# Performance work log

Measured on AMD Instinct MI355X. Metric: run time of the kernel, lower is better.

The kernel has to match this reference:

```python
import jax, jax.numpy as jnp
import numpy as np

D_MODEL = 1024
NUM_HEAD = 16


def setup_inputs() -> dict:
    key = jax.random.key(0)
    ks = jax.random.split(key, 11)
    B, S, D = 2, 2048, D_MODEL
    scale = 1.0 / np.sqrt(D)
    inp = {
        "Q": jax.random.normal(ks[0], (B, S, D), jnp.float32),
        "K": jax.random.normal(ks[1], (B, S, D), jnp.float32),
        "V": jax.random.normal(ks[2], (B, S, D), jnp.float32),
        "Wq": jax.random.normal(ks[3], (D, D), jnp.float32) * scale,
        "bq": jax.random.normal(ks[4], (D,), jnp.float32) * 0.01,
        "Wk": jax.random.normal(ks[5], (D, D), jnp.float32) * scale,
        "bk": jax.random.normal(ks[6], (D,), jnp.float32) * 0.01,
        "Wv": jax.random.normal(ks[7], (D, D), jnp.float32) * scale,
        "bv": jax.random.normal(ks[8], (D,), jnp.float32) * 0.01,
        "Wo": jax.random.normal(ks[9], (D, D), jnp.float32) * scale,
        "bo": jax.random.normal(ks[10], (D,), jnp.float32) * 0.01,
    }
    return inp


def reference(Q, K, V, Wq, bq, Wk, bk, Wv, bv, Wo, bo):
    b, vc, d_model = Q.shape
    h = NUM_HEAD
    hd = d_model // h
    # projections (torch Linear: x @ W.T + b)
    q = (Q @ Wq.T + bq).reshape(b, vc, h, hd)
    k = (K @ Wk.T + bk).reshape(b, vc, h, hd)
    v = (V @ Wv.T + bv).reshape(b, vc, h, hd)
    # scores [b,h,q,k]
    atten = jnp.einsum('bqhd,bkhd->bhqk', q, k) / np.sqrt(hd).astype(jnp.float32)
    atten = jax.nn.softmax(atten, axis=3)
    # weighted values -> [b,q,h,hd]
    out = jnp.einsum('bhqd,bdhv->bqhv', atten, v).reshape(b, vc, d_model)
    return out @ Wo.T + bo
```

## Files before the change

### kernel.cpp

```cpp
#include <hip/hip_runtime.h>

#define S_LEN 2048
#define DM 1024
#define NH 16
#define HD 64
#define NB 2

typedef unsigned short u16;
typedef __attribute__((ext_vector_type(8))) short s16x8;
typedef __attribute__((ext_vector_type(8))) unsigned short u16x8;
typedef __attribute__((ext_vector_type(4))) float fx4;
typedef __attribute__((ext_vector_type(2))) unsigned u32x2;
typedef __attribute__((ext_vector_type(4))) unsigned u32x4;

__device__ __forceinline__ u16 f2bf(float f) {
  unsigned u = __builtin_bit_cast(unsigned, f);
  return (u16)((u + 0x7FFFu + ((u >> 16) & 1u)) >> 16);
}

__device__ __forceinline__ unsigned cvt_pk_bf16(float a, float b) {
  unsigned r;
  asm("v_cvt_pk_bf16_f32 %0, %1, %2" : "=v"(r) : "v"(a), "v"(b));
  return r;
}

__device__ __forceinline__ void gload16(const void* g, void* l) {
  __builtin_amdgcn_global_load_lds(
      (const __attribute__((address_space(1))) unsigned*)g,
      (__attribute__((address_space(3))) unsigned*)l, 16, 0, 0);
}

__device__ __forceinline__ fx4 mfma16(s16x8 a, s16x8 b, fx4 c) {
  return __builtin_amdgcn_mfma_f32_16x16x32_bf16(a, b, c, 0, 0, 0);
}

__global__ __launch_bounds__(256) void cvt_w_kernel(
    const float* __restrict__ Wq, const float* __restrict__ Wk,
    const float* __restrict__ Wv, const float* __restrict__ Wo,
    u16* __restrict__ Wqb, u16* __restrict__ Wkb, u16* __restrict__ Wvb,
    u16* __restrict__ Wob) {
  const int blk = blockIdx.x;
  const float* src;
  u16* dst;
  float scale = 1.0f;
  int off;
  if (blk < 512)       { src = Wq; dst = Wqb; off = blk;        scale = 0.18033688f; }
  else if (blk < 1024) { src = Wk; dst = Wkb; off = blk - 512;  }
  else if (blk < 1536) { src = Wv; dst = Wvb; off = blk - 1024; }
  else                 { src = Wo; dst = Wob; off = blk - 1536; }
  const int i = (off * 256 + (int)threadIdx.x) * 8;
  fx4 a = *(const fx4*)(src + i);
  fx4 b = *(const fx4*)(src + i + 4);
  u16x8 o;
  o[0] = f2bf(a[0] * scale); o[1] = f2bf(a[1] * scale);
  o[2] = f2bf(a[2] * scale); o[3] = f2bf(a[3] * scale);
  o[4] = f2bf(b[0] * scale); o[5] = f2bf(b[1] * scale);
  o[6] = f2bf(b[2] * scale); o[7] = f2bf(b[3] * scale);
  *(u16x8*)(dst + i) = o;
}

__device__ __forceinline__ void store_out(u16* C, size_t idx, float v) { C[idx] = f2bf(v); }
__device__ __forceinline__ void store_out(float* C, size_t idx, float v) { C[idx] = v; }

template <typename OUT, bool AF32>
__device__ __forceinline__ void gemm_db_body(const u16* __restrict__ Abf,
                                             const float* __restrict__ Afp,
                                             const u16* __restrict__ Bt,
                                             const float* __restrict__ bias,
                                             float bscale, OUT* __restrict__ C,
                                             int m0, int n0) {
  __shared__ u16 Al[2][128 * 32];
  __shared__ u16 Bl[2][128 * 32];
  const int tid = threadIdx.x;
  const int wid = tid >> 6, lane = tid & 63;
  const int g = lane >> 4, lr = lane & 15;
  const int wr = wid >> 1, wc = wid & 1;
  const int row0 = tid >> 2, ch = tid & 3;
  const int chx = ch ^ ((row0 >> 1) & 3);
  const int wch = chx;

  fx4 acc[4][4] = {};
  fx4 pf[4];

  auto issueA = [&](int k0) {
#pragma unroll
    for (int hh = 0; hh < 2; ++hh) {
      const float* ap = Afp + (size_t)(m0 + hh * 64 + row0) * 1024 + k0 + ch * 8;
      pf[2 * hh] = *(const fx4*)ap;
      pf[2 * hh + 1] = *(const fx4*)(ap + 4);
    }
  };
  auto writeA = [&](int buf) {
#pragma unroll
    for (int hh = 0; hh < 2; ++hh) {
      u32x4 w;
      w[0] = cvt_pk_bf16(pf[2 * hh][0], pf[2 * hh][1]);
      w[1] = cvt_pk_bf16(pf[2 * hh][2], pf[2 * hh][3]);
      w[2] = cvt_pk_bf16(pf[2 * hh + 1][0], pf[2 * hh + 1][1]);
      w[3] = cvt_pk_bf16(pf[2 * hh + 1][2], pf[2 * hh + 1][3]);
      *(u32x4*)((char*)Al[buf] + hh * 4096 + row0 * 64 + wch * 16) = w;
    }
  };
  auto stage = [&](int buf, int k0) {
    if constexpr (!AF32) {
      gload16(Abf + (size_t)(m0 + row0) * 1024 + k0 + chx * 8,
              (char*)Al[buf] + wid * 1024);
      gload16(Abf + (size_t)(m0 + 64 + row0) * 1024 + k0 + chx * 8,
              (char*)Al[buf] + 4096 + wid * 1024);
    }
    gload16(Bt + (size_t)(n0 + row0) * 1024 + k0 + chx * 8,
            (char*)Bl[buf] + wid * 1024);
    gload16(Bt + (size_t)(n0 + 64 + row0) * 1024 + k0 + chx * 8,
            (char*)Bl[buf] + 4096 + wid * 1024);
  };
  auto compute = [&](int cur) {
    s16x8 a[4], b[4];
#pragma unroll
    for (int m = 0; m < 4; ++m) {
      const int row = wr * 64 + m * 16 + lr;
      a[m] = *(const s16x8*)((char*)Al[cur] + row * 64 + (g ^ ((row >> 1) & 3)) * 16);
    }
#pragma unroll
    for (int n = 0; n < 4; ++n) {
      const int row = wc * 64 + n * 16 + lr;
      b[n] = *(const s16x8*)((char*)Bl[cur] + row * 64 + (g ^ ((row >> 1) & 3)) * 16);
    }
    __builtin_amdgcn_s_setprio(1);
#pragma unroll
    for (int m = 0; m < 4; ++m)
#pragma unroll
      for (int n = 0; n < 4; ++n) acc[m][n] = mfma16(a[m], b[n], acc[m][n]);
    __builtin_amdgcn_s_setprio(0);
  };

  if constexpr (AF32) issueA(0);
  stage(0, 0);
  if constexpr (AF32) writeA(0);
  __syncthreads();

#pragma unroll 1
  for (int t = 0; t < 32; t += 2) {
    if constexpr (AF32) issueA((t + 1) * 32);
    stage(1, (t + 1) * 32);
    compute(0);
    if constexpr (AF32) writeA(1);
    __syncthreads();
    if (t + 2 < 32) {
      if constexpr (AF32) issueA((t + 2) * 32);
      stage(0, (t + 2) * 32);
    }
    compute(1);
    if (t + 2 < 32 && AF32) writeA(0);
    __syncthreads();
  }

#pragma unroll
  for (int n = 0; n < 4; ++n) {
    const int col = n0 + wc * 64 + n * 16 + lr;
    const float bv = bias[col] * bscale;
#pragma unroll
    for (int m = 0; m < 4; ++m) {
      const int row = m0 + wr * 64 + m * 16 + g * 4;
#pragma unroll
      for (int j = 0; j < 4; ++j)
        store_out(C, (size_t)(row + j) * 1024 + col, acc[m][n][j] + bv);
    }
  }
}

__global__ __launch_bounds__(256, 3) void gemm_qkv_kernel(
    const float* Q, const float* K, const float* V, const u16* Wq, const u16* Wk,
    const u16* Wv, const float* bq, const float* bk, const float* bv, u16* q,
    u16* k, u16* v) {
  const int hw = blockIdx.x + (blockIdx.y << 3) + (blockIdx.z << 8);
  const int xcd = hw & 7, j = hw >> 3;
  const int x = j & 7;
  const int p = xcd + ((j >> 3) << 3);
  const int y = p & 31, z = p >> 5;

  const float* A;
  const u16* B;
  const float* bias;
  u16* C;
  float bs;
  if (z == 0)      { A = Q; B = Wq; bias = bq; C = q; bs = 0.18033688f; }
  else if (z == 1) { A = K; B = Wk; bias = bk; C = k; bs = 1.0f; }
  else             { A = V; B = Wv; bias = bv; C = v; bs = 1.0f; }
  gemm_db_body<u16, true>(nullptr, A, B, bias, bs, C, y * 128, x * 128);
}

__global__ __launch_bounds__(256, 3) void gemm_out_kernel(const u16* ctx,
                                                          const u16* Wo,
                                                          const float* bo,
                                                          float* out) {
  const int hw = blockIdx.x + (blockIdx.y << 3);
  const int xcd = hw & 7, j = hw >> 3;
  const int x = j & 7;
  const int y = xcd + ((j >> 3) << 3);
  gemm_db_body<float, false>(ctx, nullptr, Wo, bo, 1.0f, out, y * 128, x * 128);
}

__global__ __launch_bounds__(256) void transpose_v_kernel(const u16* __restrict__ v,
                                                          u16* __restrict__ vt) {
  const int bh = blockIdx.y;
  const int b = bh >> 4, h = bh & 15;
  const int s0 = blockIdx.x * 32;
  const int d = threadIdx.x & 63;
  const int c = threadIdx.x >> 6;
  const int s = s0 + c * 8;
  const u16* src = v + ((size_t)(b * S_LEN + s)) * DM + h * HD + d;
  u16x8 o;
#pragma unroll
  for (int e = 0; e < 8; ++e) o[e] = src[(size_t)e * DM];
  *(u16x8*)(vt + ((size_t)(bh * 64 + d)) * S_LEN + s) = o;
}

__global__ __launch_bounds__(256, 4) void attn_kernel(const u16* __restrict__ qb,
                                                      const u16* __restrict__ kb,
                                                      const u16* __restrict__ vt,
                                                      u16* __restrict__ ctx) {
  __shared__ u16 Kl[2][64 * 64];
  __shared__ u16 Vl[2][64 * 64];
  __shared__ u16 Pl[4][16 * 64];

  const int tid = threadIdx.x, wid = tid >> 6, lane = tid & 63;
  const int g = lane >> 4, lr = lane & 15;
  const int rswz = (lr & 7) * 8;
  const int pswz = (lr & 7) * 16;
  char* Pb = (char*)&Pl[wid][0];
  const int bh = blockIdx.y, b = bh >> 4, h = bh & 15;
  const int q0 = blockIdx.x * 64;

  const u16* qp = qb + ((size_t)(b * S_LEN + q0 + wid * 16 + lr)) * DM + h * HD;
  s16x8 aq[2];
  aq[0] = *(const s16x8*)(qp + g * 8);
  aq[1] = *(const s16x8*)(qp + 32 + g * 8);

  fx4 accO[4] = {};
  float lrun = 0.f;

  const int srow = tid >> 3, sch = tid & 7;
  const int schx = sch ^ (srow & 7);
  const u16* kbase = kb + ((size_t)b * S_LEN) * DM + h * HD;
  const u16* vtbase = vt + ((size_t)bh * 64) * S_LEN;

#define STAGE(buf, kv)                                                             \
  do {                                                                             \
    gload16(kbase + (size_t)((kv) + srow) * DM + schx * 8,                         \
            (char*)Kl[buf] + wid * 1024);                                          \
    gload16(kbase + (size_t)((kv) + 32 + srow) * DM + schx * 8,                    \
            (char*)Kl[buf] + 4096 + wid * 1024);                                   \
    gload16(vtbase + (size_t)srow * S_LEN + (kv) + schx * 8,                       \
            (char*)Vl[buf] + wid * 1024);                                          \
    gload16(vtbase + (size_t)(32 + srow) * S_LEN + (kv) + schx * 8,                \
            (char*)Vl[buf] + 4096 + wid * 1024);                                   \
  } while (0)

  auto compute_tile = [&](const u16* Kc0, const u16* Vc0) {
    fx4 s[4] = {};
    __builtin_amdgcn_s_setprio(1);
#pragma unroll
    for (int ks = 0; ks < 2; ++ks) {
#pragma unroll
      for (int c = 0; c < 4; ++c) {
        s16x8 kf =
            *(const s16x8*)(Kc0 + (c * 16 + lr) * 64 + ((ks * 32 + g * 8) ^ rswz));
        s[c] = mfma16(kf, aq[ks], s[c]);
      }
    }
    __builtin_amdgcn_s_setprio(0);

#pragma unroll
    for (int c = 0; c < 4; ++c)
#pragma unroll
      for (int j = 0; j < 4; ++j) s[c][j] = __builtin_amdgcn_exp2f(s[c][j]);
    {
      const float r0 = (s[0][0] + s[0][1]) + (s[0][2] + s[0][3]);
      const float r1 = (s[1][0] + s[1][1]) + (s[1][2] + s[1][3]);
      const float r2 = (s[2][0] + s[2][1]) + (s[2][2] + s[2][3]);
      const float r3 = (s[3][0] + s[3][1]) + (s[3][2] + s[3][3]);
      lrun += (r0 + r1) + (r2 + r3);
    }

#pragma unroll
    for (int c = 0; c < 4; ++c) {
      u32x2 w;
      w[0] = cvt_pk_bf16(s[c][0], s[c][1]);
      w[1] = cvt_pk_bf16(s[c][2], s[c][3]);
      *(u32x2*)(Pb + lr * 128 + ((c * 32 + g * 8) ^ pswz)) = w;
    }
    asm volatile("s_waitcnt lgkmcnt(0)" ::: "memory");
    __builtin_amdgcn_sched_barrier(0);

    __builtin_amdgcn_s_setprio(1);
#pragma unroll
    for (int ks = 0; ks < 2; ++ks) {
      s16x8 pb = *(const s16x8*)(Pb + lr * 128 + ((ks * 64 + g * 16) ^ pswz));
#pragma unroll
      for (int c = 0; c < 4; ++c) {
        s16x8 vf =
            *(const s16x8*)(Vc0 + (c * 16 + lr) * 64 + ((ks * 32 + g * 8) ^ rswz));
        accO[c] = mfma16(vf, pb, accO[c]);
      }
    }
    __builtin_amdgcn_s_setprio(0);
  };

  STAGE(0, 0);
  __syncthreads();

  for (int t = 0; t < 32; t += 2) {
    if (t + 1 < 32) STAGE(1, (t + 1) * 64);
    compute_tile(Kl[0], Vl[0]);
    __syncthreads();
    if (t + 2 < 32) STAGE(0, (t + 2) * 64);
    compute_tile(Kl[1], Vl[1]);
    __syncthreads();
  }
#undef STAGE

  lrun += __shfl_xor(lrun, 16);
  lrun += __shfl_xor(lrun, 32);
  const float inv = 1.0f / lrun;
  u16* op = ctx + ((size_t)(b * S_LEN + q0 + wid * 16 + lr)) * DM + h * HD;
#pragma unroll
  for (int c = 0; c < 4; ++c) {
    u32x2 w;
    w[0] = cvt_pk_bf16(accO[c][0] * inv, accO[c][1] * inv);
    w[1] = cvt_pk_bf16(accO[c][2] * inv, accO[c][3] * inv);
    *(u32x2*)(op + c * 16 + g * 4) = w;
  }
}

extern "C" void kernel_launch(void* const* d_in, const int* in_sizes, int n_in,
                              void* d_out, int out_size, void* d_ws, size_t ws_size,
                              hipStream_t stream) {
  const float* Q = (const float*)d_in[0];
  const float* K = (const float*)d_in[1];
  const float* V = (const float*)d_in[2];
  const float* Wq = (const float*)d_in[3];
  const float* bq = (const float*)d_in[4];
  const float* Wk = (const float*)d_in[5];
  const float* bk = (const float*)d_in[6];
  const float* Wv = (const float*)d_in[7];
  const float* bv = (const float*)d_in[8];
  const float* Wo = (const float*)d_in[9];
  const float* bo = (const float*)d_in[10];
  float* out = (float*)d_out;

  char* ws = (char*)d_ws;
  const size_t SZ_T = (size_t)NB * S_LEN * DM * 2;
  const size_t SZ_W = (size_t)DM * DM * 2;

  u16* Wqb = (u16*)(ws);
  u16* Wkb = (u16*)(ws + SZ_W);
  u16* Wvb = (u16*)(ws + 2 * SZ_W);
  u16* Wob = (u16*)(ws + 3 * SZ_W);
  u16* qb  = (u16*)(ws + 4 * SZ_W);
  u16* kb  = (u16*)(ws + 4 * SZ_W + SZ_T);
  u16* vb  = (u16*)(ws + 4 * SZ_W + 2 * SZ_T);
  u16* vtb = (u16*)(ws + 4 * SZ_W + 3 * SZ_T);
  u16* ctx = (u16*)(ws + 4 * SZ_W + 4 * SZ_T);

  cvt_w_kernel<<<2048, 256, 0, stream>>>(Wq, Wk, Wv, Wo, Wqb, Wkb, Wvb, Wob);

  gemm_qkv_kernel<<<dim3(8, 32, 3), 256, 0, stream>>>(Q, K, V, Wqb, Wkb, Wvb,
                                                      bq, bk, bv, qb, kb, vb);

  transpose_v_kernel<<<dim3(64, 32), 256, 0, stream>>>(vb, vtb);

  attn_kernel<<<dim3(32, 32), 256, 0, stream>>>(qb, kb, vtb, ctx);

  gemm_out_kernel<<<dim3(8, 32), 256, 0, stream>>>(ctx, Wob, bo, out);
}
```

Baseline: 123.8 us.

## Pre-convert Q/K/V activations to bf16 in a separate pass before QKV GEMM

The QKV GEMM used to load fp32 activations through registers, convert them to bf16 and write them to LDS on every k-step. Q, K and V are now converted once in an expanded conversion kernel, so the GEMM can use direct global-to-LDS loads for both operands, as the output GEMM already does. Workspace buffers are reused for the V transpose and the context. This adds a full extra read and write pass over the activations. Separately, an explicit LDS wait and scheduling barrier in the attention kernel are removed, which may affect ordering between the P stores and the loads that follow.

```diff
diff --git a/kernel.cpp b/kernel.cpp
--- a/kernel.cpp
+++ b/kernel.cpp
@@ -11,7 +11,6 @@
 typedef __attribute__((ext_vector_type(8))) unsigned short u16x8;
 typedef __attribute__((ext_vector_type(4))) float fx4;
 typedef __attribute__((ext_vector_type(2))) unsigned u32x2;
-typedef __attribute__((ext_vector_type(4))) unsigned u32x4;
 
 __device__ __forceinline__ u16 f2bf(float f) {
   unsigned u = __builtin_bit_cast(unsigned, f);
@@ -34,20 +33,25 @@
   return __builtin_amdgcn_mfma_f32_16x16x32_bf16(a, b, c, 0, 0, 0);
 }
 
-__global__ __launch_bounds__(256) void cvt_w_kernel(
-    const float* __restrict__ Wq, const float* __restrict__ Wk,
-    const float* __restrict__ Wv, const float* __restrict__ Wo,
-    u16* __restrict__ Wqb, u16* __restrict__ Wkb, u16* __restrict__ Wvb,
-    u16* __restrict__ Wob) {
+__global__ __launch_bounds__(256) void cvt_all_kernel(
+    const float* __restrict__ Q, const float* __restrict__ K,
+    const float* __restrict__ V, const float* __restrict__ Wq,
+    const float* __restrict__ Wk, const float* __restrict__ Wv,
+    const float* __restrict__ Wo, u16* __restrict__ Qc, u16* __restrict__ Kc,
+    u16* __restrict__ Vc, u16* __restrict__ Wqb, u16* __restrict__ Wkb,
+    u16* __restrict__ Wvb, u16* __restrict__ Wob) {
   const int blk = blockIdx.x;
   const float* src;
   u16* dst;
   float scale = 1.0f;
   int off;
-  if (blk < 512)       { src = Wq; dst = Wqb; off = blk;        scale = 0.18033688f; }
-  else if (blk < 1024) { src = Wk; dst = Wkb; off = blk - 512;  }
-  else if (blk < 1536) { src = Wv; dst = Wvb; off = blk - 1024; }
-  else                 { src = Wo; dst = Wob; off = blk - 1536; }
+  if (blk < 2048)      { src = Q;  dst = Qc;  off = blk; }
+  else if (blk < 4096) { src = K;  dst = Kc;  off = blk - 2048; }
+  else if (blk < 6144) { src = V;  dst = Vc;  off = blk - 4096; }
+  else if (blk < 6656) { src = Wq; dst = Wqb; off = blk - 6144; scale = 0.18033688f; }
+  else if (blk < 7168) { src = Wk; dst = Wkb; off = blk - 6656; }
+  else if (blk < 7680) { src = Wv; dst = Wvb; off = blk - 7168; }
+  else                 { src = Wo; dst = Wob; off = blk - 7680; }
   const int i = (off * 256 + (int)threadIdx.x) * 8;
   fx4 a = *(const fx4*)(src + i);
   fx4 b = *(const fx4*)(src + i + 4);
@@ -62,9 +66,8 @@
 __device__ __forceinline__ void store_out(u16* C, size_t idx, float v) { C[idx] = f2bf(v); }
 __device__ __forceinline__ void store_out(float* C, size_t idx, float v) { C[idx] = v; }
 
-template <typename OUT, bool AF32>
-__device__ __forceinline__ void gemm_db_body(const u16* __restrict__ Abf,
-                                             const float* __restrict__ Afp,
+template <typename OUT>
+__device__ __forceinline__ void gemm_db_body(const u16* __restrict__ A,
                                              const u16* __restrict__ Bt,
                                              const float* __restrict__ bias,
                                              float bscale, OUT* __restrict__ C,
@@ -77,37 +80,14 @@
   const int wr = wid >> 1, wc = wid & 1;
   const int row0 = tid >> 2, ch = tid & 3;
   const int chx = ch ^ ((row0 >> 1) & 3);
-  const int wch = chx;
 
   fx4 acc[4][4] = {};
-  fx4 pf[4];
-
-  auto issueA = [&](int k0) {
-#pragma unroll
-    for (int hh = 0; hh < 2; ++hh) {
-      const float* ap = Afp + (size_t)(m0 + hh * 64 + row0) * 1024 + k0 + ch * 8;
-      pf[2 * hh] = *(const fx4*)ap;
-      pf[2 * hh + 1] = *(const fx4*)(ap + 4);
-    }
-  };
-  auto writeA = [&](int buf) {
-#pragma unroll
-    for (int hh = 0; hh < 2; ++hh) {
-      u32x4 w;
-      w[0] = cvt_pk_bf16(pf[2 * hh][0], pf[2 * hh][1]);
-      w[1] = cvt_pk_bf16(pf[2 * hh][2], pf[2 * hh][3]);
-      w[2] = cvt_pk_bf16(pf[2 * hh + 1][0], pf[2 * hh + 1][1]);
-      w[3] = cvt_pk_bf16(pf[2 * hh + 1][2], pf[2 * hh + 1][3]);
-      *(u32x4*)((char*)Al[buf] + hh * 4096 + row0 * 64 + wch * 16) = w;
-    }
-  };
+
   auto stage = [&](int buf, int k0) {
-    if constexpr (!AF32) {
-      gload16(Abf + (size_t)(m0 + row0) * 1024 + k0 + chx * 8,
-              (char*)Al[buf] + wid * 1024);
-      gload16(Abf + (size_t)(m0 + 64 + row0) * 1024 + k0 + chx * 8,
-              (char*)Al[buf] + 4096 + wid * 1024);
-    }
+    gload16(A + (size_t)(m0 + row0) * 1024 + k0 + chx * 8,
+            (char*)Al[buf] + wid * 1024);
+    gload16(A + (size_t)(m0 + 64 + row0) * 1024 + k0 + chx * 8,
+            (char*)Al[buf] + 4096 + wid * 1024);
     gload16(Bt + (size_t)(n0 + row0) * 1024 + k0 + chx * 8,
             (char*)Bl[buf] + wid * 1024);
     gload16(Bt + (size_t)(n0 + 64 + row0) * 1024 + k0 + chx * 8,
@@ -133,24 +113,16 @@
     __builtin_amdgcn_s_setprio(0);
   };
 
-  if constexpr (AF32) issueA(0);
   stage(0, 0);
-  if constexpr (AF32) writeA(0);
   __syncthreads();
 
 #pragma unroll 1
   for (int t = 0; t < 32; t += 2) {
-    if constexpr (AF32) issueA((t + 1) * 32);
     stage(1, (t + 1) * 32);
     compute(0);
-    if constexpr (AF32) writeA(1);
     __syncthreads();
-    if (t + 2 < 32) {
-      if constexpr (AF32) issueA((t + 2) * 32);
-      stage(0, (t + 2) * 32);
-    }
+    if (t + 2 < 32) stage(0, (t + 2) * 32);
     compute(1);
-    if (t + 2 < 32 && AF32) writeA(0);
     __syncthreads();
   }
 
@@ -169,7 +141,7 @@
 }
 
 __global__ __launch_bounds__(256, 3) void gemm_qkv_kernel(
-    const float* Q, const float* K, const float* V, const u16* Wq, const u16* Wk,
+    const u16* Qc, const u16* Kc, const u16* Vc, const u16* Wq, const u16* Wk,
     const u16* Wv, const float* bq, const float* bk, const float* bv, u16* q,
     u16* k, u16* v) {
   const int hw = blockIdx.x + (blockIdx.y << 3) + (blockIdx.z << 8);
@@ -178,15 +150,15 @@
   const int p = xcd + ((j >> 3) << 3);
   const int y = p & 31, z = p >> 5;
 
-  const float* A;
+  const u16* A;
   const u16* B;
   const float* bias;
   u16* C;
   float bs;
-  if (z == 0)      { A = Q; B = Wq; bias = bq; C = q; bs = 0.18033688f; }
-  else if (z == 1) { A = K; B = Wk; bias = bk; C = k; bs = 1.0f; }
-  else             { A = V; B = Wv; bias = bv; C = v; bs = 1.0f; }
-  gemm_db_body<u16, true>(nullptr, A, B, bias, bs, C, y * 128, x * 128);
+  if (z == 0)      { A = Qc; B = Wq; bias = bq; C = q; bs = 0.18033688f; }
+  else if (z == 1) { A = Kc; B = Wk; bias = bk; C = k; bs = 1.0f; }
+  else             { A = Vc; B = Wv; bias = bv; C = v; bs = 1.0f; }
+  gemm_db_body<u16>(A, B, bias, bs, C, y * 128, x * 128);
 }
 
 __global__ __launch_bounds__(256, 3) void gemm_out_kernel(const u16* ctx,
@@ -197,7 +169,7 @@
   const int xcd = hw & 7, j = hw >> 3;
   const int x = j & 7;
   const int y = xcd + ((j >> 3) << 3);
-  gemm_db_body<float, false>(ctx, nullptr, Wo, bo, 1.0f, out, y * 128, x * 128);
+  gemm_db_body<float>(ctx, Wo, bo, 1.0f, out, y * 128, x * 128);
 }
 
 __global__ __launch_bounds__(256) void transpose_v_kernel(const u16* __restrict__ v,
@@ -289,8 +261,6 @@
       w[1] = cvt_pk_bf16(s[c][2], s[c][3]);
       *(u32x2*)(Pb + lr * 128 + ((c * 32 + g * 8) ^ pswz)) = w;
     }
-    asm volatile("s_waitcnt lgkmcnt(0)" ::: "memory");
-    __builtin_amdgcn_sched_barrier(0);
 
     __builtin_amdgcn_s_setprio(1);
 #pragma unroll
@@ -356,15 +326,19 @@
   u16* Wkb = (u16*)(ws + SZ_W);
   u16* Wvb = (u16*)(ws + 2 * SZ_W);
   u16* Wob = (u16*)(ws + 3 * SZ_W);
-  u16* qb  = (u16*)(ws + 4 * SZ_W);
-  u16* kb  = (u16*)(ws + 4 * SZ_W + SZ_T);
-  u16* vb  = (u16*)(ws + 4 * SZ_W + 2 * SZ_T);
-  u16* vtb = (u16*)(ws + 4 * SZ_W + 3 * SZ_T);
-  u16* ctx = (u16*)(ws + 4 * SZ_W + 4 * SZ_T);
-
-  cvt_w_kernel<<<2048, 256, 0, stream>>>(Wq, Wk, Wv, Wo, Wqb, Wkb, Wvb, Wob);
-
-  gemm_qkv_kernel<<<dim3(8, 32, 3), 256, 0, stream>>>(Q, K, V, Wqb, Wkb, Wvb,
+  u16* Qc  = (u16*)(ws + 4 * SZ_W);
+  u16* Kc  = (u16*)(ws + 4 * SZ_W + SZ_T);
+  u16* Vc  = (u16*)(ws + 4 * SZ_W + 2 * SZ_T);
+  u16* qb  = (u16*)(ws + 4 * SZ_W + 3 * SZ_T);
+  u16* kb  = (u16*)(ws + 4 * SZ_W + 4 * SZ_T);
+  u16* vb  = (u16*)(ws + 4 * SZ_W + 5 * SZ_T);
+  u16* vtb = Qc;
+  u16* ctx = Kc;
+
+  cvt_all_kernel<<<8192, 256, 0, stream>>>(Q, K, V, Wq, Wk, Wv, Wo, Qc, Kc, Vc,
+                                           Wqb, Wkb, Wvb, Wob);
+
+  gemm_qkv_kernel<<<dim3(8, 32, 3), 256, 0, stream>>>(Qc, Kc, Vc, Wqb, Wkb, Wvb,
                                                       bq, bk, bv, qb, kb, vb);
 
   transpose_v_kernel<<<dim3(64, 32), 256, 0, stream>>>(vb, vtb);
```

Result: slower. 130.5 us (+5.4%).

## Split attention KV tile across waves, keep P in registers, cross-wave reduce

Applied to the files above, without the earlier changes.

The attention kernel now gives each block 32 query rows, and each wave handles 16 keys of every 64-key tile instead of 16 queries against all keys. Because the score accumulator layout directly feeds a 16x16x16 bf16 MFMA, the P tile is passed in registers and the LDS round trip for P goes away. Partial outputs and row sums are reduced across the four waves through shared memory at the end. The grid becomes a 1D launch of 2048 blocks that groups heads by XCD for L2 locality. In exchange, each block loads K/V tiles for fewer queries, doubling K/V traffic per query, and the kernel adds an end-of-kernel LDS reduction.

```diff
diff --git a/kernel.cpp b/kernel.cpp
--- a/kernel.cpp
+++ b/kernel.cpp
@@ -8,6 +8,7 @@
 
 typedef unsigned short u16;
 typedef __attribute__((ext_vector_type(8))) short s16x8;
+typedef __attribute__((ext_vector_type(4))) short s16x4;
 typedef __attribute__((ext_vector_type(8))) unsigned short u16x8;
 typedef __attribute__((ext_vector_type(4))) float fx4;
 typedef __attribute__((ext_vector_type(2))) unsigned u32x2;
@@ -32,6 +33,18 @@
 
 __device__ __forceinline__ fx4 mfma16(s16x8 a, s16x8 b, fx4 c) {
   return __builtin_amdgcn_mfma_f32_16x16x32_bf16(a, b, c, 0, 0, 0);
+}
+
+__device__ __forceinline__ fx4 mfma16k16(s16x4 a, s16x4 b, fx4 c) {
+#if __has_builtin(__builtin_amdgcn_mfma_f32_16x16x16bf16_1k)
+  return __builtin_amdgcn_mfma_f32_16x16x16bf16_1k(a, b, c, 0, 0, 0);
+#else
+  fx4 d;
+  asm volatile("v_mfma_f32_16x16x16_bf16 %0, %1, %2, %3"
+               : "=v"(d)
+               : "v"(a), "v"(b), "v"(c));
+  return d;
+#endif
 }
 
 __global__ __launch_bounds__(256) void cvt_w_kernel(
@@ -219,89 +232,81 @@
                                                       const u16* __restrict__ kb,
                                                       const u16* __restrict__ vt,
                                                       u16* __restrict__ ctx) {
-  __shared__ u16 Kl[2][64 * 64];
-  __shared__ u16 Vl[2][64 * 64];
-  __shared__ u16 Pl[4][16 * 64];
+  __shared__ __align__(16) char smem[34304];
+#define KBUF(bf) ((char*)smem + (bf) * 8192)
+#define VBUF(bf) ((char*)smem + 16384 + (bf) * 8192)
 
   const int tid = threadIdx.x, wid = tid >> 6, lane = tid & 63;
   const int g = lane >> 4, lr = lane & 15;
   const int rswz = (lr & 7) * 8;
-  const int pswz = (lr & 7) * 16;
-  char* Pb = (char*)&Pl[wid][0];
-  const int bh = blockIdx.y, b = bh >> 4, h = bh & 15;
-  const int q0 = blockIdx.x * 64;
-
-  const u16* qp = qb + ((size_t)(b * S_LEN + q0 + wid * 16 + lr)) * DM + h * HD;
-  s16x8 aq[2];
-  aq[0] = *(const s16x8*)(qp + g * 8);
-  aq[1] = *(const s16x8*)(qp + 32 + g * 8);
-
-  fx4 accO[4] = {};
-  float lrun = 0.f;
+  const int w16 = wid * 16;
+
+  const int hw = blockIdx.x;
+  const int xcd = hw & 7, slot = hw >> 3;
+  const int bh = xcd * 4 + (slot >> 6);
+  const int b = bh >> 4, h = bh & 15;
+  const int q0 = (slot & 63) * 32;
+
+  const u16* qp = qb + ((size_t)(b * S_LEN + q0 + lr)) * DM + h * HD;
+  s16x8 aq[2][2];
+#pragma unroll
+  for (int qg = 0; qg < 2; ++qg) {
+    aq[qg][0] = *(const s16x8*)(qp + (size_t)qg * 16 * DM + g * 8);
+    aq[qg][1] = *(const s16x8*)(qp + (size_t)qg * 16 * DM + 32 + g * 8);
+  }
+
+  fx4 accO0[4] = {}, accO1[4] = {};
+  float lrun0 = 0.f, lrun1 = 0.f;
 
   const int srow = tid >> 3, sch = tid & 7;
   const int schx = sch ^ (srow & 7);
   const u16* kbase = kb + ((size_t)b * S_LEN) * DM + h * HD;
   const u16* vtbase = vt + ((size_t)bh * 64) * S_LEN;
 
-#define STAGE(buf, kv)                                                             \
+#define STAGE(bf, kv)                                                              \
   do {                                                                             \
-    gload16(kbase + (size_t)((kv) + srow) * DM + schx * 8,                         \
-            (char*)Kl[buf] + wid * 1024);                                          \
+    gload16(kbase + (size_t)((kv) + srow) * DM + schx * 8, KBUF(bf) + wid * 1024); \
     gload16(kbase + (size_t)((kv) + 32 + srow) * DM + schx * 8,                    \
-            (char*)Kl[buf] + 4096 + wid * 1024);                                   \
+            KBUF(bf) + 4096 + wid * 1024);                                         \
     gload16(vtbase + (size_t)srow * S_LEN + (kv) + schx * 8,                       \
-            (char*)Vl[buf] + wid * 1024);                                          \
+            VBUF(bf) + wid * 1024);                                                \
     gload16(vtbase + (size_t)(32 + srow) * S_LEN + (kv) + schx * 8,                \
-            (char*)Vl[buf] + 4096 + wid * 1024);                                   \
+            VBUF(bf) + 4096 + wid * 1024);                                         \
   } while (0)
 
+  const int voff = ((((wid << 1) | (g >> 1)) ^ (lr & 7)) << 3) + ((g & 1) << 2);
+
   auto compute_tile = [&](const u16* Kc0, const u16* Vc0) {
-    fx4 s[4] = {};
+    s16x8 kf0 = *(const s16x8*)(Kc0 + (w16 + lr) * 64 + ((g * 8) ^ rswz));
+    s16x8 kf1 = *(const s16x8*)(Kc0 + (w16 + lr) * 64 + ((32 + g * 8) ^ rswz));
+    fx4 s0 = {}, s1 = {};
     __builtin_amdgcn_s_setprio(1);
-#pragma unroll
-    for (int ks = 0; ks < 2; ++ks) {
-#pragma unroll
-      for (int c = 0; c < 4; ++c) {
-        s16x8 kf =
-            *(const s16x8*)(Kc0 + (c * 16 + lr) * 64 + ((ks * 32 + g * 8) ^ rswz));
-        s[c] = mfma16(kf, aq[ks], s[c]);
-      }
-    }
+    s0 = mfma16(kf0, aq[0][0], s0);
+    s1 = mfma16(kf0, aq[1][0], s1);
+    s0 = mfma16(kf1, aq[0][1], s0);
+    s1 = mfma16(kf1, aq[1][1], s1);
     __builtin_amdgcn_s_setprio(0);
 
 #pragma unroll
-    for (int c = 0; c < 4; ++c)
-#pragma unroll
-      for (int j = 0; j < 4; ++j) s[c][j] = __builtin_amdgcn_exp2f(s[c][j]);
-    {
-      const float r0 = (s[0][0] + s[0][1]) + (s[0][2] + s[0][3]);
-      const float r1 = (s[1][0] + s[1][1]) + (s[1][2] + s[1][3]);
-      const float r2 = (s[2][0] + s[2][1]) + (s[2][2] + s[2][3]);
-      const float r3 = (s[3][0] + s[3][1]) + (s[3][2] + s[3][3]);
-      lrun += (r0 + r1) + (r2 + r3);
-    }
-
+    for (int j = 0; j < 4; ++j) {
+      s0[j] = __builtin_amdgcn_exp2f(s0[j]);
+      s1[j] = __builtin_amdgcn_exp2f(s1[j]);
+    }
+    lrun0 += (s0[0] + s0[1]) + (s0[2] + s0[3]);
+    lrun1 += (s1[0] + s1[1]) + (s1[2] + s1[3]);
+
+    u32x2 p0, p1;
+    p0[0] = cvt_pk_bf16(s0[0], s0[1]); p0[1] = cvt_pk_bf16(s0[2], s0[3]);
+    p1[0] = cvt_pk_bf16(s1[0], s1[1]); p1[1] = cvt_pk_bf16(s1[2], s1[3]);
+    const s16x4 pb0 = __builtin_bit_cast(s16x4, p0);
+    const s16x4 pb1 = __builtin_bit_cast(s16x4, p1);
+
+    __builtin_amdgcn_s_setprio(1);
 #pragma unroll
     for (int c = 0; c < 4; ++c) {
-      u32x2 w;
-      w[0] = cvt_pk_bf16(s[c][0], s[c][1]);
-      w[1] = cvt_pk_bf16(s[c][2], s[c][3]);
-      *(u32x2*)(Pb + lr * 128 + ((c * 32 + g * 8) ^ pswz)) = w;
-    }
-    asm volatile("s_waitcnt lgkmcnt(0)" ::: "memory");
-    __builtin_amdgcn_sched_barrier(0);
-
-    __builtin_amdgcn_s_setprio(1);
-#pragma unroll
-    for (int ks = 0; ks < 2; ++ks) {
-      s16x8 pb = *(const s16x8*)(Pb + lr * 128 + ((ks * 64 + g * 16) ^ pswz));
-#pragma unroll
-      for (int c = 0; c < 4; ++c) {
-        s16x8 vf =
-            *(const s16x8*)(Vc0 + (c * 16 + lr) * 64 + ((ks * 32 + g * 8) ^ rswz));
-        accO[c] = mfma16(vf, pb, accO[c]);
-      }
+      s16x4 vf = *(const s16x4*)(Vc0 + (c * 16 + lr) * 64 + voff);
+      accO0[c] = mfma16k16(vf, pb0, accO0[c]);
+      accO1[c] = mfma16k16(vf, pb1, accO1[c]);
     }
     __builtin_amdgcn_s_setprio(0);
   };
@@ -311,25 +316,55 @@
 
   for (int t = 0; t < 32; t += 2) {
     if (t + 1 < 32) STAGE(1, (t + 1) * 64);
-    compute_tile(Kl[0], Vl[0]);
+    compute_tile((const u16*)KBUF(0), (const u16*)VBUF(0));
     __syncthreads();
     if (t + 2 < 32) STAGE(0, (t + 2) * 64);
-    compute_tile(Kl[1], Vl[1]);
+    compute_tile((const u16*)KBUF(1), (const u16*)VBUF(1));
     __syncthreads();
   }
 #undef STAGE
 
-  lrun += __shfl_xor(lrun, 16);
-  lrun += __shfl_xor(lrun, 32);
-  const float inv = 1.0f / lrun;
-  u16* op = ctx + ((size_t)(b * S_LEN + q0 + wid * 16 + lr)) * DM + h * HD;
-#pragma unroll
-  for (int c = 0; c < 4; ++c) {
-    u32x2 w;
-    w[0] = cvt_pk_bf16(accO[c][0] * inv, accO[c][1] * inv);
-    w[1] = cvt_pk_bf16(accO[c][2] * inv, accO[c][3] * inv);
-    *(u32x2*)(op + c * 16 + g * 4) = w;
-  }
+  __syncthreads();
+  float* redf = (float*)smem;
+  {
+    const int rb = wid * 2112 + lane * 33;
+#pragma unroll
+    for (int c = 0; c < 4; ++c)
+#pragma unroll
+      for (int r = 0; r < 4; ++r) {
+        redf[rb + c * 4 + r] = accO0[c][r];
+        redf[rb + 16 + c * 4 + r] = accO1[c][r];
+      }
+  }
+  lrun0 += __shfl_xor(lrun0, 16); lrun0 += __shfl_xor(lrun0, 32);
+  lrun1 += __shfl_xor(lrun1, 16); lrun1 += __shfl_xor(lrun1, 32);
+  if (lane < 16) {
+    redf[8448 + wid * 16 + lane] = lrun0;
+    redf[8512 + wid * 16 + lane] = lrun1;
+  }
+  __syncthreads();
+  const float inv0 = 1.0f / (redf[8448 + lr] + redf[8464 + lr] +
+                             redf[8480 + lr] + redf[8496 + lr]);
+  const float inv1 = 1.0f / (redf[8512 + lr] + redf[8528 + lr] +
+                             redf[8544 + lr] + redf[8560 + lr]);
+
+  u16* op = ctx + ((size_t)(b * S_LEN + q0 + lr)) * DM + h * HD + wid * 16 + g * 4;
+#pragma unroll
+  for (int qg = 0; qg < 2; ++qg) {
+    float v0 = 0.f, v1 = 0.f, v2 = 0.f, v3 = 0.f;
+#pragma unroll
+    for (int u = 0; u < 4; ++u) {
+      const float* p = redf + u * 2112 + lane * 33 + qg * 16 + wid * 4;
+      v0 += p[0]; v1 += p[1]; v2 += p[2]; v3 += p[3];
+    }
+    const float inv = qg ? inv1 : inv0;
+    u32x2 wv;
+    wv[0] = cvt_pk_bf16(v0 * inv, v1 * inv);
+    wv[1] = cvt_pk_bf16(v2 * inv, v3 * inv);
+    *(u32x2*)(op + (size_t)qg * 16 * DM) = wv;
+  }
+#undef KBUF
+#undef VBUF
 }
 
 extern "C" void kernel_launch(void* const* d_in, const int* in_sizes, int n_in,
@@ -369,7 +404,7 @@
 
   transpose_v_kernel<<<dim3(64, 32), 256, 0, stream>>>(vb, vtb);
 
-  attn_kernel<<<dim3(32, 32), 256, 0, stream>>>(qb, kb, vtb, ctx);
+  attn_kernel<<<2048, 256, 0, stream>>>(qb, kb, vtb, ctx);
 
   gemm_out_kernel<<<dim3(8, 32), 256, 0, stream>>>(ctx, Wob, bo, out);
 }
```

New measurement: 129.7 us. 4.7% more time.
